# Kernel tuning notes

Measured on AMD Instinct MI355X. Metric: run time of the kernel, lower is better.

## Reference

```python
import jax, jax.numpy as jnp
import numpy as np
from jax import lax

B, D, T = 32, 2048, 512

def setup_inputs() -> dict:
    key = jax.random.key(0)
    k1, k2 = jax.random.split(key)
    input_spikes = jax.random.normal(k1, (B, D, T), dtype=jnp.float32)
    # alpha_1 = exp(-1/tau) per feature; original uses a constant tau but the
    # parameter is trainable, so treat it as a learned per-feature coefficient in (0,1).
    alpha = jax.random.uniform(k2, (D,), dtype=jnp.float32)
    return {"input_spikes": input_spikes, "alpha": alpha}

def reference(input_spikes, alpha):
    """First-order low-pass (EMA) filter: s_t = alpha * s_{t-1} + x_t.
    input_spikes: [B, D, T]; alpha: [D]. Returns (psp [B,D,T], final_state [B,D]).
    """
    x_t = jnp.moveaxis(input_spikes, -1, 0)  # [T, B, D]
    init = jnp.zeros(input_spikes.shape[:-1], dtype=input_spikes.dtype)  # [B, D]

    def step(state, xt):
        s = alpha * state + xt
        return s, s

    final_state, ys = lax.scan(step, init, x_t)
    psp = jnp.moveaxis(ys, 0, -1)  # [B, D, T]
    return psp, final_state
```

## Files before the change

### kernel.cpp

```cpp
#include <hip/hip_runtime.h>


#define BB 32
#define DD 2048
#define TT 512
#define NSEQ (BB * DD)

__global__ __launch_bounds__(256) void ema_scan_kernel(
    const float* __restrict__ x,
    const float* __restrict__ alpha_arr,
    float* __restrict__ psp,
    float* __restrict__ final_state)
{
    const int gtid = blockIdx.x * 256 + threadIdx.x;
    const int seq  = gtid >> 6;
    const int lane = threadIdx.x & 63;
    if (seq >= NSEQ) return;

    const int d = seq & (DD - 1);
    const float alpha = alpha_arr[d];

    const float* xp = x + (size_t)seq * TT + (size_t)lane * 8;

    float4 v0 = *reinterpret_cast<const float4*>(xp);
    float4 v1 = *reinterpret_cast<const float4*>(xp + 4);

    float y0 = v0.x;
    float y1 = fmaf(alpha, y0, v0.y);
    float y2 = fmaf(alpha, y1, v0.z);
    float y3 = fmaf(alpha, y2, v0.w);
    float y4 = fmaf(alpha, y3, v1.x);
    float y5 = fmaf(alpha, y4, v1.y);
    float y6 = fmaf(alpha, y5, v1.z);
    float y7 = fmaf(alpha, y6, v1.w);

    const float a2 = alpha * alpha;
    const float a4 = a2 * a2;
    float A  = a4 * a4;
    float Bc = y7;

    #pragma unroll
    for (int off = 1; off < 64; off <<= 1) {
        float aP = __shfl_up(A,  off);
        float bP = __shfl_up(Bc, off);
        if (lane >= off) {
            Bc = fmaf(A, bP, Bc);
            A  = A * aP;
        }
    }

    float s_in = __shfl_up(Bc, 1);
    if (lane == 0) s_in = 0.0f;

    float pw = alpha;
    y0 = fmaf(pw, s_in, y0); pw *= alpha;
    y1 = fmaf(pw, s_in, y1); pw *= alpha;
    y2 = fmaf(pw, s_in, y2); pw *= alpha;
    y3 = fmaf(pw, s_in, y3); pw *= alpha;
    y4 = fmaf(pw, s_in, y4); pw *= alpha;
    y5 = fmaf(pw, s_in, y5); pw *= alpha;
    y6 = fmaf(pw, s_in, y6); pw *= alpha;
    y7 = fmaf(pw, s_in, y7);

    float* op = psp + (size_t)seq * TT + (size_t)lane * 8;
    *reinterpret_cast<float4*>(op)     = make_float4(y0, y1, y2, y3);
    *reinterpret_cast<float4*>(op + 4) = make_float4(y4, y5, y6, y7);

    if (lane == 63) {
        final_state[seq] = y7;
    }
}

extern "C" void kernel_launch(void* const* d_in, const int* in_sizes, int n_in,
                              void* d_out, int out_size, void* d_ws, size_t ws_size,
                              hipStream_t stream) {
    const float* x     = (const float*)d_in[0];
    const float* alpha = (const float*)d_in[1];
    float* psp         = (float*)d_out;
    float* final_state = (float*)d_out + (size_t)NSEQ * TT;

    const int blocks = NSEQ / 4;
    ema_scan_kernel<<<blocks, 256, 0, stream>>>(x, alpha, psp, final_state);
}
```

Measured before the change: 46.60 us.

## Process four sequences per wavefront with interleaved scans and nontemporal stores

Each wavefront now handles four sequences instead of one. Their loads, local scans and cross-lane shuffle scans are interleaved, which gives more independent work to hide shuffle latency and cuts the block count by four. Outputs are written with nontemporal stores, and the final state is written as one vector store. Per-thread register use goes up and the grid becomes smaller, which may reduce occupancy and latency hiding for this memory-bound kernel.

```diff
diff --git a/kernel.cpp b/kernel.cpp
--- a/kernel.cpp
+++ b/kernel.cpp
@@ -5,69 +5,104 @@
 #define DD 2048
 #define TT 512
 #define NSEQ (BB * DD)
+#define SPW 4
 
-__global__ __launch_bounds__(256) void ema_scan_kernel(
+typedef float f32x4 __attribute__((ext_vector_type(4)));
+
+__global__ __launch_bounds__(256) void ema_scan4_kernel(
     const float* __restrict__ x,
     const float* __restrict__ alpha_arr,
     float* __restrict__ psp,
     float* __restrict__ final_state)
 {
     const int gtid = blockIdx.x * 256 + threadIdx.x;
-    const int seq  = gtid >> 6;
+    const int wave = gtid >> 6;
     const int lane = threadIdx.x & 63;
-    if (seq >= NSEQ) return;
+    const int seq0 = wave * SPW;
+    if (seq0 >= NSEQ) return;
 
-    const int d = seq & (DD - 1);
-    const float alpha = alpha_arr[d];
+    const int d0 = seq0 & (DD - 1);
+    const f32x4 al4 = *reinterpret_cast<const f32x4*>(alpha_arr + d0);
+    const float alpha[SPW] = {al4.x, al4.y, al4.z, al4.w};
 
-    const float* xp = x + (size_t)seq * TT + (size_t)lane * 8;
+    const float* xp = x + (size_t)seq0 * TT + (size_t)lane * 8;
 
-    float4 v0 = *reinterpret_cast<const float4*>(xp);
-    float4 v1 = *reinterpret_cast<const float4*>(xp + 4);
+    f32x4 v[SPW][2];
+    #pragma unroll
+    for (int s = 0; s < SPW; ++s) {
+        v[s][0] = *reinterpret_cast<const f32x4*>(xp + (size_t)s * TT);
+        v[s][1] = *reinterpret_cast<const f32x4*>(xp + (size_t)s * TT + 4);
+    }
 
-    float y0 = v0.x;
-    float y1 = fmaf(alpha, y0, v0.y);
-    float y2 = fmaf(alpha, y1, v0.z);
-    float y3 = fmaf(alpha, y2, v0.w);
-    float y4 = fmaf(alpha, y3, v1.x);
-    float y5 = fmaf(alpha, y4, v1.y);
-    float y6 = fmaf(alpha, y5, v1.z);
-    float y7 = fmaf(alpha, y6, v1.w);
+    float y[SPW][8];
+    #pragma unroll
+    for (int s = 0; s < SPW; ++s) {
+        const float a = alpha[s];
+        y[s][0] = v[s][0].x;
+        y[s][1] = fmaf(a, y[s][0], v[s][0].y);
+        y[s][2] = fmaf(a, y[s][1], v[s][0].z);
+        y[s][3] = fmaf(a, y[s][2], v[s][0].w);
+        y[s][4] = fmaf(a, y[s][3], v[s][1].x);
+        y[s][5] = fmaf(a, y[s][4], v[s][1].y);
+        y[s][6] = fmaf(a, y[s][5], v[s][1].z);
+        y[s][7] = fmaf(a, y[s][6], v[s][1].w);
+    }
 
-    const float a2 = alpha * alpha;
-    const float a4 = a2 * a2;
-    float A  = a4 * a4;
-    float Bc = y7;
+    float A[SPW], Bc[SPW];
+    #pragma unroll
+    for (int s = 0; s < SPW; ++s) {
+        const float a2 = alpha[s] * alpha[s];
+        const float a4 = a2 * a2;
+        A[s]  = a4 * a4;
+        Bc[s] = y[s][7];
+    }
 
     #pragma unroll
     for (int off = 1; off < 64; off <<= 1) {
-        float aP = __shfl_up(A,  off);
-        float bP = __shfl_up(Bc, off);
+        float aP[SPW], bP[SPW];
+        #pragma unroll
+        for (int s = 0; s < SPW; ++s) {
+            aP[s] = __shfl_up(A[s],  off);
+            bP[s] = __shfl_up(Bc[s], off);
+        }
         if (lane >= off) {
-            Bc = fmaf(A, bP, Bc);
-            A  = A * aP;
+            #pragma unroll
+            for (int s = 0; s < SPW; ++s) {
+                Bc[s] = fmaf(A[s], bP[s], Bc[s]);
+                A[s]  = A[s] * aP[s];
+            }
         }
     }
 
-    float s_in = __shfl_up(Bc, 1);
-    if (lane == 0) s_in = 0.0f;
+    float s_in[SPW];
+    #pragma unroll
+    for (int s = 0; s < SPW; ++s) {
+        float t = __shfl_up(Bc[s], 1);
+        s_in[s] = (lane == 0) ? 0.0f : t;
+    }
 
-    float pw = alpha;
-    y0 = fmaf(pw, s_in, y0); pw *= alpha;
-    y1 = fmaf(pw, s_in, y1); pw *= alpha;
-    y2 = fmaf(pw, s_in, y2); pw *= alpha;
-    y3 = fmaf(pw, s_in, y3); pw *= alpha;
-    y4 = fmaf(pw, s_in, y4); pw *= alpha;
-    y5 = fmaf(pw, s_in, y5); pw *= alpha;
-    y6 = fmaf(pw, s_in, y6); pw *= alpha;
-    y7 = fmaf(pw, s_in, y7);
+    #pragma unroll
+    for (int s = 0; s < SPW; ++s) {
+        float pw = alpha[s];
+        #pragma unroll
+        for (int j = 0; j < 8; ++j) {
+            y[s][j] = fmaf(pw, s_in[s], y[s][j]);
+            pw *= alpha[s];
+        }
+    }
 
-    float* op = psp + (size_t)seq * TT + (size_t)lane * 8;
-    *reinterpret_cast<float4*>(op)     = make_float4(y0, y1, y2, y3);
-    *reinterpret_cast<float4*>(op + 4) = make_float4(y4, y5, y6, y7);
+    float* op = psp + (size_t)seq0 * TT + (size_t)lane * 8;
+    #pragma unroll
+    for (int s = 0; s < SPW; ++s) {
+        f32x4 o0 = {y[s][0], y[s][1], y[s][2], y[s][3]};
+        f32x4 o1 = {y[s][4], y[s][5], y[s][6], y[s][7]};
+        __builtin_nontemporal_store(o0, reinterpret_cast<f32x4*>(op + (size_t)s * TT));
+        __builtin_nontemporal_store(o1, reinterpret_cast<f32x4*>(op + (size_t)s * TT + 4));
+    }
 
     if (lane == 63) {
-        final_state[seq] = y7;
+        f32x4 fs = {y[0][7], y[1][7], y[2][7], y[3][7]};
+        *reinterpret_cast<f32x4*>(final_state + seq0) = fs;
     }
 }
 
@@ -79,6 +114,6 @@
     float* psp         = (float*)d_out;
     float* final_state = (float*)d_out + (size_t)NSEQ * TT;
 
-    const int blocks = NSEQ / 4;
-    ema_scan_kernel<<<blocks, 256, 0, stream>>>(x, alpha, psp, final_state);
+    const int blocks = NSEQ / (SPW * 4);
+    ema_scan4_kernel<<<blocks, 256, 0, stream>>>(x, alpha, psp, final_state);
 }
```

Result: slower. 84.45 us (+81.2%).
